# Performance work log

Measured on AMD Instinct MI355X. Metric: run time of the kernel, lower is better.

## Reference

```python
import jax, jax.numpy as jnp
import numpy as np

# FlowNetC correlation config (matches init_kwargs)
PAD = 20           # pad_size
MAX_DISP = 20      # max_displacement
STRIDE2 = 2        # displacement stride
K = 1              # kernel_size (1x1 patch)
# stride1 = 1, corr_multiply = 1 (multiply mode)

GRID_RAD = MAX_DISP // STRIDE2           # 10
N_DISP = (2 * GRID_RAD + 1) ** 2         # 441 output channels


def _disp_offsets():
    # slice start offsets into the padded input2 for each displacement
    # (dy, dx) in {-GRID_RAD..GRID_RAD} * STRIDE2; start = PAD + d (pad == max_disp)
    d = np.arange(-GRID_RAD, GRID_RAD + 1) * STRIDE2
    dy, dx = np.meshgrid(d, d, indexing='ij')  # row-major: dy outer, dx inner
    return np.stack([PAD + dy.ravel(), PAD + dx.ravel()], axis=1).astype(np.int32)  # [441,2]


def setup_inputs() -> dict:
    key = jax.random.key(0)
    k1, k2 = jax.random.split(key)
    B, C, H, W = 8, 256, 64, 64
    input1 = jax.random.normal(k1, (B, C, H, W), dtype=jnp.float32)
    input2 = jax.random.normal(k2, (B, C, H, W), dtype=jnp.float32)
    return {"input1": input1, "input2": input2}


def reference(input1, input2):
    B, C, H, W = input1.shape
    sumelems = float(K * K * C)  # normalization used by the CUDA kernel
    # zero-pad input2 spatially by PAD (pad_size == max_displacement)
    x2p = jnp.pad(input2, ((0, 0), (0, 0), (PAD, PAD), (PAD, PAD)))
    offs = jnp.asarray(_disp_offsets())  # [441, 2] int32

    def step(carry, off):
        # window of input2 displaced by (dy, dx) relative to input1
        sl = jax.lax.dynamic_slice(x2p, (0, 0, off[0], off[1]), (B, C, H, W))
        corr = jnp.sum(input1 * sl, axis=1) / sumelems  # [B, H, W]
        return carry, corr

    _, out = jax.lax.scan(step, None, offs)       # [441, B, H, W]
    return jnp.transpose(out, (1, 0, 2, 3))       # [B, 441, H, W]
```

## Files before the change

kernel.cpp:

```cpp
#include <hip/hip_runtime.h>
#include <hip/hip_bf16.h>


typedef short    bf16x8 __attribute__((ext_vector_type(8)));
typedef float    f32x4  __attribute__((ext_vector_type(4)));
typedef unsigned u32x2  __attribute__((ext_vector_type(2)));

constexpr int CSTRIDE = 64 * 64;
constexpr int BSTRIDE = 256 * CSTRIDE;
constexpr int NCOLS   = 112;
constexpr int CSTR    = 134;

union BF2 { __hip_bfloat162 h; unsigned u; };
union BF1 { __hip_bfloat16 h; unsigned short u; };

__device__ inline unsigned pack_bf2(float lo, float hi) {
    BF2 cv;
    cv.h = __float22bfloat162_rn(make_float2(lo, hi));
    return cv.u;
}

__global__ __launch_bounds__(256)
void conv_in2(const float* __restrict__ in2, unsigned short* __restrict__ in2t)
{
    __shared__ unsigned short lt[64 * 66];
    const int tid = threadIdx.x;
    const int b = blockIdx.x & 7;
    const int y = blockIdx.x >> 3;
    const float* src = in2 + b * BSTRIDE + y * 64;
    unsigned* odw = reinterpret_cast<unsigned*>(in2t + (b * 64 + y) * (64 * 256));

    for (int c0 = 0; c0 < 256; c0 += 64) {
        __syncthreads();
#pragma unroll
        for (int it = 0; it < 16; ++it) {
            const int c = it * 4 + (tid >> 6);
            const int x = tid & 63;
            BF1 cv; cv.h = __float2bfloat16(src[(c0 + c) * CSTRIDE + x]);
            lt[x * 66 + c] = cv.u;
        }
        __syncthreads();
        const unsigned* ldw = reinterpret_cast<const unsigned*>(lt);
#pragma unroll
        for (int it = 0; it < 8; ++it) {
            const int flat = tid + 256 * it;
            const int x  = flat >> 5;
            const int cp = flat & 31;
            odw[x * 128 + (c0 >> 1) + cp] = ldw[x * 33 + cp];
        }
    }
}

__global__ __launch_bounds__(512, 4)
void corr_mfma(const float* __restrict__ in1,
               const unsigned short* __restrict__ in2t,
               float* __restrict__ out)
{
    __shared__ __align__(16) unsigned blds[NCOLS * CSTR];
    __shared__ float slds[21 * 65];

    const int tid  = threadIdx.x;
    const int lane = tid & 63;
    const int w    = tid >> 6;
    const int b    = blockIdx.x & 7;
    const int y    = blockIdx.x >> 3;

    const int cl = lane & 15;
    const int q  = lane >> 4;
    const int m  = w & 3;
    const int nh = w >> 2;

    const float* i1b = in1 + b * BSTRIDE;

    bf16x8 afrag[8];
#pragma unroll
    for (int k = 0; k < 8; ++k) {
        const float* p = i1b + (32 * k + 8 * q) * CSTRIDE + y * 64 + 16 * m + cl;
        float v[8];
#pragma unroll
        for (int j = 0; j < 8; ++j) v[j] = p[j * CSTRIDE];
#pragma unroll
        for (int j = 0; j < 4; ++j)
            ((unsigned*)&afrag[k])[j] = pack_bf2(v[2 * j], v[2 * j + 1]);
    }

    for (int i = tid; i < 48 * 128; i += 512) {
        const int colz = i >> 7;
        const int col  = (colz < 20) ? colz : colz + 64;
        blds[col * CSTR + (i & 127)] = 0u;
    }

    for (int r = 0; r < 21; ++r) {
        const int yy = y + 2 * r - 20;
        const int ob = (b * 441 + r * 21) * CSTRIDE + y * 64;

        if (yy < 0 || yy > 63) {
            for (int i = tid; i < 21 * 64; i += 512)
                out[ob + (i >> 6) * CSTRIDE + (i & 63)] = 0.f;
            continue;
        }

        {
            const uint4* src = reinterpret_cast<const uint4*>(
                in2t + (b * 64 + yy) * (64 * 256));
#pragma unroll
            for (int j = 0; j < 4; ++j) {
                const int seg = tid + 512 * j;
                const int x   = seg >> 5;
                const int cw  = (seg & 31) << 2;
                const uint4 v = src[seg];
                unsigned* d = &blds[(x + 20) * CSTR + cw];
                *reinterpret_cast<u32x2*>(d)     = u32x2{v.x, v.y};
                *reinterpret_cast<u32x2*>(d + 2) = u32x2{v.z, v.w};
            }
        }
        __syncthreads();

#pragma unroll
        for (int nn = 0; nn < 2; ++nn) {
            const int n     = m + 2 * nh + nn;
            const int baddr = (16 * n + cl) * CSTR + 4 * q;
            f32x4 acc = {0.f, 0.f, 0.f, 0.f};
#pragma unroll
            for (int k = 0; k < 8; ++k) {
                bf16x8 bfrag;
                ((u32x2*)&bfrag)[0] = *(const u32x2*)&blds[baddr + 16 * k];
                ((u32x2*)&bfrag)[1] = *(const u32x2*)&blds[baddr + 16 * k + 2];
                acc = __builtin_amdgcn_mfma_f32_16x16x32_bf16(afrag[k], bfrag, acc, 0, 0, 0);
            }
            const int gcol = 16 * n + cl;
#pragma unroll
            for (int i = 0; i < 4; ++i) {
                const int gx = 16 * m + 4 * q + i;
                const int d2 = gcol - gx;
                if (d2 >= 0 && d2 <= 40 && !(d2 & 1))
                    slds[(d2 >> 1) * 65 + gx] = acc[i];
            }
        }
        __syncthreads();

        for (int i = tid; i < 21 * 64; i += 512) {
            const int dx = i >> 6, gx = i & 63;
            out[ob + dx * CSTRIDE + gx] = slds[dx * 65 + gx] * (1.f / 256.f);
        }
        __syncthreads();
    }
}

extern "C" void kernel_launch(void* const* d_in, const int* in_sizes, int n_in,
                              void* d_out, int out_size, void* d_ws, size_t ws_size,
                              hipStream_t stream) {
    const float* in1 = (const float*)d_in[0];
    const float* in2 = (const float*)d_in[1];
    float* out = (float*)d_out;
    unsigned short* in2t = (unsigned short*)d_ws;

    conv_in2<<<dim3(512), dim3(256), 0, stream>>>(in2, in2t);
    corr_mfma<<<dim3(512), dim3(512), 0, stream>>>(in1, in2t, out);
}
```

Before: 154.6 us.

## Pair two output rows per block and load MFMA B fragments directly from global

The conv_in2 output layout changes to an 8-channel-group-major bf16 format, so each lane can fetch its MFMA B fragment as one aligned 16-byte global load. This removes the LDS staging of input2 rows and its barrier. Each block now handles two output rows (y0 and y0+2) that share the same displaced input2 rows, so every B fragment feeds two MFMAs. Block size doubles to 1024 threads and the grid halves, which raises register pressure (two A-fragment sets) and relies on L2/L1 for the B reuse that LDS used to provide.

```diff
diff --git a/kernel.cpp b/kernel.cpp
--- a/kernel.cpp
+++ b/kernel.cpp
@@ -4,12 +4,9 @@
 
 typedef short    bf16x8 __attribute__((ext_vector_type(8)));
 typedef float    f32x4  __attribute__((ext_vector_type(4)));
-typedef unsigned u32x2  __attribute__((ext_vector_type(2)));
 
 constexpr int CSTRIDE = 64 * 64;
 constexpr int BSTRIDE = 256 * CSTRIDE;
-constexpr int NCOLS   = 112;
-constexpr int CSTR    = 134;
 
 union BF2 { __hip_bfloat162 h; unsigned u; };
 union BF1 { __hip_bfloat16 h; unsigned short u; };
@@ -20,15 +17,17 @@
     return cv.u;
 }
 
+__device__ __align__(16) const uint4 ZERO16 = {0u, 0u, 0u, 0u};
+
 __global__ __launch_bounds__(256)
-void conv_in2(const float* __restrict__ in2, unsigned short* __restrict__ in2t)
+void conv_in2(const float* __restrict__ in2, unsigned* __restrict__ out_dw)
 {
     __shared__ unsigned short lt[64 * 66];
     const int tid = threadIdx.x;
     const int b = blockIdx.x & 7;
     const int y = blockIdx.x >> 3;
     const float* src = in2 + b * BSTRIDE + y * 64;
-    unsigned* odw = reinterpret_cast<unsigned*>(in2t + (b * 64 + y) * (64 * 256));
+    unsigned* odw = out_dw + (b * 64 + y) * 8192;
 
     for (int c0 = 0; c0 < 256; c0 += 64) {
         __syncthreads();
@@ -43,105 +42,97 @@
         const unsigned* ldw = reinterpret_cast<const unsigned*>(lt);
 #pragma unroll
         for (int it = 0; it < 8; ++it) {
-            const int flat = tid + 256 * it;
-            const int x  = flat >> 5;
-            const int cp = flat & 31;
-            odw[x * 128 + (c0 >> 1) + cp] = ldw[x * 33 + cp];
+            const int d   = tid + 256 * it;
+            const int c8g = d >> 8;
+            const int x   = (d >> 2) & 63;
+            const int cd2 = d & 3;
+            odw[((c0 >> 3) + c8g) * 256 + x * 4 + cd2] = ldw[x * 33 + c8g * 4 + cd2];
         }
     }
 }
 
-__global__ __launch_bounds__(512, 4)
+__global__ __launch_bounds__(1024, 4)
 void corr_mfma(const float* __restrict__ in1,
-               const unsigned short* __restrict__ in2t,
+               const uint4* __restrict__ in2t,
                float* __restrict__ out)
 {
-    __shared__ __align__(16) unsigned blds[NCOLS * CSTR];
-    __shared__ float slds[21 * 65];
+    __shared__ float slds[2][21 * 65];
 
     const int tid  = threadIdx.x;
     const int lane = tid & 63;
     const int w    = tid >> 6;
+    const int cl   = lane & 15;
+    const int q    = lane >> 4;
+    const int m    = w & 3;
+    const int n    = m + (w >> 2);
     const int b    = blockIdx.x & 7;
-    const int y    = blockIdx.x >> 3;
+    const int p    = blockIdx.x >> 3;
+    const int y0   = 4 * (p >> 1) + (p & 1);
 
-    const int cl = lane & 15;
-    const int q  = lane >> 4;
-    const int m  = w & 3;
-    const int nh = w >> 2;
-
-    const float* i1b = in1 + b * BSTRIDE;
-
-    bf16x8 afrag[8];
+    bf16x8 af[2][8];
 #pragma unroll
-    for (int k = 0; k < 8; ++k) {
-        const float* p = i1b + (32 * k + 8 * q) * CSTRIDE + y * 64 + 16 * m + cl;
-        float v[8];
+    for (int h = 0; h < 2; ++h) {
+        const float* pb = in1 + b * BSTRIDE + (y0 + 2 * h) * 64 + 16 * m + cl
+                        + 8 * q * CSTRIDE;
 #pragma unroll
-        for (int j = 0; j < 8; ++j) v[j] = p[j * CSTRIDE];
+        for (int k = 0; k < 8; ++k) {
+            const float* pp = pb + 32 * k * CSTRIDE;
+            float v[8];
 #pragma unroll
-        for (int j = 0; j < 4; ++j)
-            ((unsigned*)&afrag[k])[j] = pack_bf2(v[2 * j], v[2 * j + 1]);
+            for (int j = 0; j < 8; ++j) v[j] = pp[j * CSTRIDE];
+#pragma unroll
+            for (int j = 0; j < 4; ++j)
+                ((unsigned*)&af[h][k])[j] = pack_bf2(v[2 * j], v[2 * j + 1]);
+        }
     }
 
-    for (int i = tid; i < 48 * 128; i += 512) {
-        const int colz = i >> 7;
-        const int col  = (colz < 20) ? colz : colz + 64;
-        blds[col * CSTR + (i & 127)] = 0u;
-    }
+    const int  x    = 16 * n + cl - 20;
+    const bool xok  = (x >= 0) && (x < 64);
+    const int  gcol = 16 * n + cl;
 
-    for (int r = 0; r < 21; ++r) {
-        const int yy = y + 2 * r - 20;
-        const int ob = (b * 441 + r * 21) * CSTRIDE + y * 64;
+    for (int i = 0; i < 22; ++i) {
+        const int  yy      = y0 - 20 + 2 * i;
+        const bool compute = (yy >= 0) && (yy < 64);
 
-        if (yy < 0 || yy > 63) {
-            for (int i = tid; i < 21 * 64; i += 512)
-                out[ob + (i >> 6) * CSTRIDE + (i & 63)] = 0.f;
-            continue;
-        }
-
-        {
-            const uint4* src = reinterpret_cast<const uint4*>(
-                in2t + (b * 64 + yy) * (64 * 256));
+        if (compute) {
+            const uint4* src = in2t + (b * 64 + yy) * 2048 + x;
+            f32x4 acc0 = {0.f, 0.f, 0.f, 0.f};
+            f32x4 acc1 = {0.f, 0.f, 0.f, 0.f};
 #pragma unroll
-            for (int j = 0; j < 4; ++j) {
-                const int seg = tid + 512 * j;
-                const int x   = seg >> 5;
-                const int cw  = (seg & 31) << 2;
-                const uint4 v = src[seg];
-                unsigned* d = &blds[(x + 20) * CSTR + cw];
-                *reinterpret_cast<u32x2*>(d)     = u32x2{v.x, v.y};
-                *reinterpret_cast<u32x2*>(d + 2) = u32x2{v.z, v.w};
+            for (int k = 0; k < 8; ++k) {
+                const uint4* pk = xok ? (src + (4 * k + q) * 64) : &ZERO16;
+                const uint4  wv = *pk;
+                const bf16x8 bf = __builtin_bit_cast(bf16x8, wv);
+                acc0 = __builtin_amdgcn_mfma_f32_16x16x32_bf16(af[0][k], bf, acc0, 0, 0, 0);
+                acc1 = __builtin_amdgcn_mfma_f32_16x16x32_bf16(af[1][k], bf, acc1, 0, 0, 0);
+            }
+#pragma unroll
+            for (int i4 = 0; i4 < 4; ++i4) {
+                const int gx = 16 * m + 4 * q + i4;
+                const int d2 = gcol - gx;
+                if (d2 >= 0 && d2 <= 40 && !(d2 & 1)) {
+                    slds[0][(d2 >> 1) * 65 + gx] = acc0[i4];
+                    slds[1][(d2 >> 1) * 65 + gx] = acc1[i4];
+                }
             }
         }
         __syncthreads();
 
+        const int r0 = i, r1 = i - 1;
 #pragma unroll
-        for (int nn = 0; nn < 2; ++nn) {
-            const int n     = m + 2 * nh + nn;
-            const int baddr = (16 * n + cl) * CSTR + 4 * q;
-            f32x4 acc = {0.f, 0.f, 0.f, 0.f};
-#pragma unroll
-            for (int k = 0; k < 8; ++k) {
-                bf16x8 bfrag;
-                ((u32x2*)&bfrag)[0] = *(const u32x2*)&blds[baddr + 16 * k];
-                ((u32x2*)&bfrag)[1] = *(const u32x2*)&blds[baddr + 16 * k + 2];
-                acc = __builtin_amdgcn_mfma_f32_16x16x32_bf16(afrag[k], bfrag, acc, 0, 0, 0);
+        for (int t3 = 0; t3 < 3; ++t3) {
+            const int t = tid + 1024 * t3;
+            if (t < 2 * 21 * 64) {
+                const int h  = (t >= 1344) ? 1 : 0;
+                const int u  = t - 1344 * h;
+                const int dx = u >> 6, gx = u & 63;
+                const int r  = h ? r1 : r0;
+                if (r >= 0 && r <= 20) {
+                    const float val = compute ? slds[h][dx * 65 + gx] * (1.f / 256.f)
+                                              : 0.f;
+                    out[((b * 441 + r * 21 + dx) * 64 + y0 + 2 * h) * 64 + gx] = val;
+                }
             }
-            const int gcol = 16 * n + cl;
-#pragma unroll
-            for (int i = 0; i < 4; ++i) {
-                const int gx = 16 * m + 4 * q + i;
-                const int d2 = gcol - gx;
-                if (d2 >= 0 && d2 <= 40 && !(d2 & 1))
-                    slds[(d2 >> 1) * 65 + gx] = acc[i];
-            }
-        }
-        __syncthreads();
-
-        for (int i = tid; i < 21 * 64; i += 512) {
-            const int dx = i >> 6, gx = i & 63;
-            out[ob + dx * CSTRIDE + gx] = slds[dx * 65 + gx] * (1.f / 256.f);
         }
         __syncthreads();
     }
@@ -153,8 +144,7 @@
     const float* in1 = (const float*)d_in[0];
     const float* in2 = (const float*)d_in[1];
     float* out = (float*)d_out;
-    unsigned short* in2t = (unsigned short*)d_ws;
 
-    conv_in2<<<dim3(512), dim3(256), 0, stream>>>(in2, in2t);
-    corr_mfma<<<dim3(512), dim3(512), 0, stream>>>(in1, in2t, out);
+    conv_in2<<<dim3(512), dim3(256), 0, stream>>>(in2, (unsigned*)d_ws);
+    corr_mfma<<<dim3(256), dim3(1024), 0, stream>>>(in1, (const uint4*)d_ws, out);
 }
```

After: 151.1 us. -2.3%, faster.
